# Performance work log

Hardware: AMD Instinct MI355X
Metric: run time of the kernel (lower is better)

The kernel has to match this reference:

```python
import jax, jax.numpy as jnp
import numpy as np

B, NV, NRINGS, NDIRS, C, F = 2, 20000, 8, 8, 16, 16


def setup_inputs() -> dict:
    key = jax.random.key(0)
    ks = jax.random.split(key, 7)
    y = jax.random.normal(ks[0], (B, NV, NDIRS, C), jnp.float32)
    contributors = jax.random.randint(ks[1], (NV, NRINGS, NDIRS, 3), 0, NV, dtype=jnp.int32)
    weights_bary = jax.random.uniform(ks[2], (NV, NRINGS, NDIRS, 3), jnp.float32)
    angles = jax.random.randint(ks[3], (NV, NRINGS, NDIRS, 3), 0, NDIRS, dtype=jnp.int32)
    kernel = jax.random.normal(ks[4], (NRINGS, NDIRS, C, F), jnp.float32) * 0.05
    center_kernel = jax.random.normal(ks[5], (C, F), jnp.float32) * 0.05
    bias = jnp.zeros((F,), jnp.float32)
    return {"y": y, "contributors": contributors, "weights_bary": weights_bary,
            "angles": angles, "kernel": kernel, "center_kernel": center_kernel, "bias": bias}


def reference(y, contributors, weights_bary, angles, kernel, center_kernel, bias):
    # y: (B, nv, ndirs, C); tables: (nv, nrings, ndirs, 3)
    b, nv, ndirs, nch = y.shape
    nfilters = kernel.shape[-1]
    nrings = contributors.shape[1]

    # window_interpolation_sync: gather 3 contributor vertices per window bin,
    # with the direction axis re-indexed per-contributor (radial sync), then
    # barycentric-weighted sum.  Flatten (vertex, dir) into one gather index.
    idx = contributors * ndirs + angles                 # (nv, nrings, ndirs, 3)
    y_flat = y.reshape(b, nv * ndirs, nch)
    gathered = y_flat[:, idx, :]                        # (B, nv, nrings, ndirs, 3, C)
    z = jnp.einsum('bvrdjc,vrdj->bvrdc', gathered, weights_bary)  # (B, nv, nrings, ndirs, C)

    # gcnn_conv: circular pad over dirs then VALID conv with (nrings, ndirs) kernel
    zr = z.reshape(b * nv, nrings, ndirs, nch)
    zr = jnp.concatenate([zr, zr[:, :, :-1, :]], axis=2)  # width 2*ndirs-1
    conv = jax.lax.conv_general_dilated(
        zr, kernel, window_strides=(1, 1), padding='VALID',
        dimension_numbers=('NHWC', 'HWIO', 'NHWC'))       # (B*nv, 1, ndirs, F)
    conv = conv.reshape(b, nv, ndirs, nfilters)

    out = conv + jnp.einsum('bvdc,cf->bvdf', y, center_kernel) + bias
    out = jax.nn.relu(out)
    return jnp.max(out, axis=2)                          # take_max over directions -> (B, nv, F)
```

## Files before the change

### kernel.cpp

```cpp
#include <hip/hip_runtime.h>

typedef unsigned short u16;
typedef __attribute__((ext_vector_type(4))) unsigned int u32x4;
typedef __attribute__((ext_vector_type(4))) float f32x4;
typedef __attribute__((ext_vector_type(8))) __bf16 bf16x8;

constexpr int BATCH = 2;
constexpr int NV    = 20000;
constexpr int ND    = 8;
constexpr int CH    = 16;
constexpr int NF    = 16;
constexpr int NVD   = NV * ND;
constexpr int NCHUNK = 36;
constexpr int MTOT  = BATCH * NV;
constexpr int BSTR  = 40;
constexpr int KSPLIT_CH = 18;
constexpr int PREP_BLOCKS = 1250;
constexpr int K2_BLOCKS   = (NCHUNK * 4096) / 256;

constexpr size_t Y16_OFF_B = 0;
constexpr size_t K2C_OFF_B = 10240000;
constexpr size_t PB_OFF_B  = 10534912;

__device__ __forceinline__ u16 f2bf(float x) {
    unsigned int u = __float_as_uint(x);
    unsigned int r = (u + 0x7fffu + ((u >> 16) & 1u)) >> 16;
    return (u16)r;
}
__device__ __forceinline__ unsigned int pack2bf(float a, float b) {
    return (unsigned int)f2bf(a) | ((unsigned int)f2bf(b) << 16);
}

__global__ __launch_bounds__(256) void prep_k2(const float* __restrict__ y,
                                               u16* __restrict__ y16,
                                               const float* __restrict__ kern,
                                               const float* __restrict__ ck,
                                               u16* __restrict__ k2c) {
    int bid = blockIdx.x;
    if (bid < PREP_BLOCKS) {
        int tid = bid * 256 + threadIdx.x;
        const float4* src = (const float4*)(y + (size_t)tid * 16);
        float4 v0 = src[0], v1 = src[1], v2 = src[2], v3 = src[3];
        u32x4 lo = {pack2bf(v0.x, v0.y), pack2bf(v0.z, v0.w), pack2bf(v1.x, v1.y), pack2bf(v1.z, v1.w)};
        u32x4 hi = {pack2bf(v2.x, v2.y), pack2bf(v2.z, v2.w), pack2bf(v3.x, v3.y), pack2bf(v3.z, v3.w)};
        u16* yd = y16 + (size_t)tid * 16;
        *(u32x4*)(yd)     = lo;
        *(u32x4*)(yd + 8) = hi;
    } else {
        int e = (bid - PREP_BLOCKS) * 256 + threadIdx.x;
        int i = e & 4095;
        int kc = e >> 12;
        int n = i >> 5, kk = i & 31;
        int k = kc * 32 + kk;
        int w = n >> 4, f = n & 15;
        float val;
        if (k < 1024) {
            int r = k >> 7, dd = (k >> 4) & 7, c = k & 15;
            int d = (dd - w) & 7;
            val = kern[((r * 8 + d) * 16 + c) * 16 + f];
        } else {
            int ke = k - 1024;
            int d = ke >> 4, c = ke & 15;
            val = (d == w) ? ck[c * 16 + f] : 0.f;
        }
        k2c[e] = f2bf(val);
    }
}

__global__ __launch_bounds__(256) void fused_gather_gemm(const u16* __restrict__ y16,
                                                         const int* __restrict__ contrib,
                                                         const float* __restrict__ wbary,
                                                         const int* __restrict__ angles,
                                                         const u16* __restrict__ k2c,
                                                         float* __restrict__ pb) {
    __shared__ __align__(16) u16 Bb[2][128 * BSTR];
    const int t = threadIdx.x;
    const int s  = blockIdx.x & 1;
    const int kcBeg = s * KSPLIT_CH;
    const int kcEnd = kcBeg + KSPLIT_CH;
    const int w = t >> 6, lane = t & 63;
    const int lrow = lane & 15, lq = lane >> 4;
    const int s_p = lq >> 1;
    const int h8  = (lq & 1) * 8;
    const int m0 = (blockIdx.x >> 1) * 64;
    const int arow = m0 + w * 16 + lrow;
    const int b_p = (arow >= NV);
    const int v_p = arow - b_p * NV;
    const u16* __restrict__ yb = y16 + (size_t)b_p * NVD * CH + h8;
    const int mb0 = v_p * 192 + s_p * 3;
    const int sn = t >> 1, sh = (t & 1) * 16;

    int   cA0, cA1, cA2, aA0, aA1, aA2;  float wA0, wA1, wA2, vA0, vA1, vA2;  u32x4 gA0, gA1, gA2;
    int   cB0, cB1, cB2, aB0, aB1, aB2;  float wB0, wB1, wB2, vB0, vB1, vB2;  u32x4 gB0, gB1, gB2;
    int   cC0, cC1, cC2, aC0, aC1, aC2;  float wC0, wC1, wC2, vC0, vC1, vC2;  u32x4 gC0, gC1, gC2;
    u32x4 bne0, bne1, bno0, bno1;

    f32x4 acc[8];
    #pragma unroll
    for (int nt = 0; nt < 8; ++nt) acc[nt] = (f32x4){0.f, 0.f, 0.f, 0.f};

#define META_ISSUE(S, KC_) { const int o_ = mb0 + (KC_) * 6;                       \
    c##S##0 = contrib[o_]; c##S##1 = contrib[o_ + 1]; c##S##2 = contrib[o_ + 2];   \
    a##S##0 = angles[o_];  a##S##1 = angles[o_ + 1];  a##S##2 = angles[o_ + 2];    \
    w##S##0 = wbary[o_];   w##S##1 = wbary[o_ + 1];   w##S##2 = wbary[o_ + 2]; }

#define G_ISSUE(S, KC_) {                                                          \
    if ((KC_) < 32) {                                                              \
        g##S##0 = *(const u32x4*)(yb + (size_t)((unsigned)c##S##0 * 128u +         \
                                                (unsigned)a##S##0 * 16u));         \
        g##S##1 = *(const u32x4*)(yb + (size_t)((unsigned)c##S##1 * 128u +         \
                                                (unsigned)a##S##1 * 16u));         \
        g##S##2 = *(const u32x4*)(yb + (size_t)((unsigned)c##S##2 * 128u +         \
                                                (unsigned)a##S##2 * 16u));         \
        v##S##0 = w##S##0; v##S##1 = w##S##1; v##S##2 = w##S##2;                   \
    } else {                                                                       \
        g##S##0 = *(const u32x4*)(yb + (size_t)((unsigned)v_p * 128u +             \
                                      (unsigned)(2 * ((KC_) - 32) + s_p) * 16u));  \
    } }

#define COMBINE(S, KC_, A_) {                                                      \
    if ((KC_) < 32) {                                                              \
        float ac_[8];                                                              \
        _Pragma("unroll") for (int x_ = 0; x_ < 8; ++x_) ac_[x_] = 0.f;            \
        _Pragma("unroll")                                                          \
        for (int q_ = 0; q_ < 4; ++q_) {                                           \
            unsigned u0_ = g##S##0[q_], u1_ = g##S##1[q_], u2_ = g##S##2[q_];      \
            ac_[2 * q_]     += v##S##0 * __uint_as_float(u0_ << 16);               \
            ac_[2 * q_ + 1] += v##S##0 * __uint_as_float(u0_ & 0xffff0000u);       \
            ac_[2 * q_]     += v##S##1 * __uint_as_float(u1_ << 16);               \
            ac_[2 * q_ + 1] += v##S##1 * __uint_as_float(u1_ & 0xffff0000u);       \
            ac_[2 * q_]     += v##S##2 * __uint_as_float(u2_ << 16);               \
            ac_[2 * q_ + 1] += v##S##2 * __uint_as_float(u2_ & 0xffff0000u);       \
        }                                                                          \
        u32x4 o_;                                                                  \
        _Pragma("unroll") for (int q_ = 0; q_ < 4; ++q_)                           \
            o_[q_] = pack2bf(ac_[2 * q_], ac_[2 * q_ + 1]);                        \
        A_ = *(bf16x8*)&o_;                                                        \
    } else { u32x4 o_ = g##S##0; A_ = *(bf16x8*)&o_; } }

#define CHUNK_EV(S, KC_) {                                                              \
    __syncthreads();                                                                    \
    if ((KC_) + 2 < kcEnd) {                                                            \
        const u32x4* src_ = (const u32x4*)(k2c + (size_t)((KC_) + 2) * 4096 + sn * 32 + sh); \
        bne0 = src_[0]; bne1 = src_[1];                                                 \
    }                                                                                   \
    bf16x8 av_;                                                                         \
    COMBINE(S, KC_, av_);                                                               \
    if ((KC_) + 3 < kcEnd) G_ISSUE(S, (KC_) + 3);                                       \
    if ((KC_) + 6 < kcEnd && (KC_) + 6 < 32) META_ISSUE(S, (KC_) + 6);                  \
    {   bf16x8 bf_[8];                                                                  \
        _Pragma("unroll")                                                               \
        for (int nt_ = 0; nt_ < 8; ++nt_)                                               \
            bf_[nt_] = *(const bf16x8*)(&Bb[0][(nt_ * 16 + lrow) * BSTR + lq * 8]);     \
        _Pragma("unroll")                                                               \
        for (int nt_ = 0; nt_ < 8; ++nt_)                                               \
            acc[nt_] = __builtin_amdgcn_mfma_f32_16x16x32_bf16(av_, bf_[nt_], acc[nt_], 0, 0, 0); \
    }                                                                                   \
    if ((KC_) + 1 < kcEnd) {                                                            \
        u16* dst_ = &Bb[1][sn * BSTR + sh];                                             \
        *(u32x4*)(dst_)     = bno0;                                                     \
        *(u32x4*)(dst_ + 8) = bno1;                                                     \
    } }

#define CHUNK_OD(S, KC_) {                                                              \
    __syncthreads();                                                                    \
    if ((KC_) + 2 < kcEnd) {                                                            \
        const u32x4* src_ = (const u32x4*)(k2c + (size_t)((KC_) + 2) * 4096 + sn * 32 + sh); \
        bno0 = src_[0]; bno1 = src_[1];                                                 \
    }                                                                                   \
    bf16x8 av_;                                                                         \
    COMBINE(S, KC_, av_);                                                               \
    if ((KC_) + 3 < kcEnd) G_ISSUE(S, (KC_) + 3);                                       \
    if ((KC_) + 6 < kcEnd && (KC_) + 6 < 32) META_ISSUE(S, (KC_) + 6);                  \
    {   bf16x8 bf_[8];                                                                  \
        _Pragma("unroll")                                                               \
        for (int nt_ = 0; nt_ < 8; ++nt_)                                               \
            bf_[nt_] = *(const bf16x8*)(&Bb[1][(nt_ * 16 + lrow) * BSTR + lq * 8]);     \
        _Pragma("unroll")                                                               \
        for (int nt_ = 0; nt_ < 8; ++nt_)                                               \
            acc[nt_] = __builtin_amdgcn_mfma_f32_16x16x32_bf16(av_, bf_[nt_], acc[nt_], 0, 0, 0); \
    }                                                                                   \
    if ((KC_) + 1 < kcEnd) {                                                            \
        u16* dst_ = &Bb[0][sn * BSTR + sh];                                             \
        *(u32x4*)(dst_)     = bne0;                                                     \
        *(u32x4*)(dst_ + 8) = bne1;                                                     \
    } }

    META_ISSUE(A, kcBeg + 0);
    META_ISSUE(B, kcBeg + 1);
    META_ISSUE(C, kcBeg + 2);
    {
        const u32x4* src = (const u32x4*)(k2c + (size_t)kcBeg * 4096 + sn * 32 + sh);
        u32x4 b0 = src[0], b1 = src[1];
        u16* dst = &Bb[0][sn * BSTR + sh];
        *(u32x4*)(dst)     = b0;
        *(u32x4*)(dst + 8) = b1;
    }
    G_ISSUE(A, kcBeg + 0); META_ISSUE(A, kcBeg + 3);
    G_ISSUE(B, kcBeg + 1); META_ISSUE(B, kcBeg + 4);
    G_ISSUE(C, kcBeg + 2); META_ISSUE(C, kcBeg + 5);
    {
        const u32x4* src = (const u32x4*)(k2c + (size_t)(kcBeg + 1) * 4096 + sn * 32 + sh);
        bno0 = src[0]; bno1 = src[1];
    }

    for (int p = 0; p < 3; ++p) {
        const int base = kcBeg + 6 * p;
        CHUNK_EV(A, base + 0);
        CHUNK_OD(B, base + 1);
        CHUNK_EV(C, base + 2);
        CHUNK_OD(A, base + 3);
        CHUNK_EV(B, base + 4);
        CHUNK_OD(C, base + 5);
    }
#undef META_ISSUE
#undef G_ISSUE
#undef COMBINE
#undef CHUNK_EV
#undef CHUNK_OD

    float* pbs = pb + (size_t)(s * 128) * MTOT;
    #pragma unroll
    for (int nt = 0; nt < 8; ++nt) {
        *(f32x4*)(pbs + (size_t)(nt * 16 + lrow) * MTOT + m0 + w * 16 + lq * 4) = acc[nt];
    }
}

__global__ __launch_bounds__(256) void combine_max(const float* __restrict__ pb,
                                                   const float* __restrict__ bias,
                                                   float* __restrict__ out) {
    int tid = blockIdx.x * 256 + threadIdx.x;
    if (tid >= 2 * MTOT) return;
    int row = tid >> 1, half = tid & 1;
    const float* p0 = pb + row;
    const float* p1 = pb + (size_t)128 * MTOT + row;
    float bs[8], m[8];
    #pragma unroll
    for (int j = 0; j < 8; ++j) { bs[j] = bias[half * 8 + j]; m[j] = 0.f; }
    #pragma unroll
    for (int w = 0; w < 8; ++w) {
        #pragma unroll
        for (int j = 0; j < 8; ++j) {
            int n = w * 16 + half * 8 + j;
            float v = p0[(size_t)n * MTOT] + p1[(size_t)n * MTOT] + bs[j];
            m[j] = fmaxf(m[j], v);
        }
    }
    float4 o0 = {m[0], m[1], m[2], m[3]};
    float4 o1 = {m[4], m[5], m[6], m[7]};
    float* dst = out + (size_t)row * NF + half * 8;
    *(float4*)(dst)     = o0;
    *(float4*)(dst + 4) = o1;
}

extern "C" void kernel_launch(void* const* d_in, const int* in_sizes, int n_in,
                              void* d_out, int out_size, void* d_ws, size_t ws_size,
                              hipStream_t stream) {
    const float* y      = (const float*)d_in[0];
    const int*   contrib= (const int*)d_in[1];
    const float* wbary  = (const float*)d_in[2];
    const int*   angles = (const int*)d_in[3];
    const float* kern   = (const float*)d_in[4];
    const float* ck     = (const float*)d_in[5];
    const float* bias   = (const float*)d_in[6];
    float* out = (float*)d_out;

    u16*   y16 = (u16*)((char*)d_ws + Y16_OFF_B);
    u16*   k2c = (u16*)((char*)d_ws + K2C_OFF_B);
    float* pb  = (float*)((char*)d_ws + PB_OFF_B);

    prep_k2<<<PREP_BLOCKS + K2_BLOCKS, 256, 0, stream>>>(y, y16, kern, ck, k2c);
    fused_gather_gemm<<<2 * (MTOT / 64), 256, 0, stream>>>(y16, contrib, wbary, angles,
                                                           k2c, pb);
    combine_max<<<(2 * MTOT + 255) / 256, 256, 0, stream>>>(pb, bias, out);
}
```

Baseline: 239.8 us.

## Precompute gather offsets and stage metadata through LDS with XCD-aware block mapping

A new prep pass fuses contributors and angles into a single precomputed element offset table. The GEMM kernel now loads that offset table and the barycentric weights cooperatively in coalesced int2/float2 form into double-buffered shared memory, so per-lane strided scalar metadata loads go away. Work items are remapped so each XCD's blocks handle one batch, which should keep that batch's y16 slice in the local L2. The cost is an extra 15MB write and read of the offset table in the prep kernel and extra LDS traffic and barriers.

```diff
diff --git a/kernel.cpp b/kernel.cpp
--- a/kernel.cpp
+++ b/kernel.cpp
@@ -15,12 +15,16 @@
 constexpr int MTOT  = BATCH * NV;
 constexpr int BSTR  = 40;
 constexpr int KSPLIT_CH = 18;
+constexpr int TPB   = 313;
+constexpr int ITEMS_PB = TPB * 2;
 constexpr int PREP_BLOCKS = 1250;
-constexpr int K2_BLOCKS   = (NCHUNK * 4096) / 256;
-
-constexpr size_t Y16_OFF_B = 0;
-constexpr size_t K2C_OFF_B = 10240000;
-constexpr size_t PB_OFF_B  = 10534912;
+constexpr int K2_BLOCKS   = 576;
+constexpr int MIDX_BLOCKS = 7500;
+
+constexpr size_t Y16_OFF_B  = 0;
+constexpr size_t K2C_OFF_B  = 10240000;
+constexpr size_t MIDX_OFF_B = 10534912;
+constexpr size_t PB_OFF_B   = 25894912;
 
 __device__ __forceinline__ u16 f2bf(float x) {
     unsigned int u = __float_as_uint(x);
@@ -35,7 +39,10 @@
                                                u16* __restrict__ y16,
                                                const float* __restrict__ kern,
                                                const float* __restrict__ ck,
-                                               u16* __restrict__ k2c) {
+                                               u16* __restrict__ k2c,
+                                               const int* __restrict__ contrib,
+                                               const int* __restrict__ angles,
+                                               int* __restrict__ midx) {
     int bid = blockIdx.x;
     if (bid < PREP_BLOCKS) {
         int tid = bid * 256 + threadIdx.x;
@@ -46,7 +53,7 @@
         u16* yd = y16 + (size_t)tid * 16;
         *(u32x4*)(yd)     = lo;
         *(u32x4*)(yd + 8) = hi;
-    } else {
+    } else if (bid < PREP_BLOCKS + K2_BLOCKS) {
         int e = (bid - PREP_BLOCKS) * 256 + threadIdx.x;
         int i = e & 4095;
         int kc = e >> 12;
@@ -64,59 +71,85 @@
             val = (d == w) ? ck[c * 16 + f] : 0.f;
         }
         k2c[e] = f2bf(val);
+    } else {
+        size_t k = (size_t)(bid - (PREP_BLOCKS + K2_BLOCKS)) * 256 + threadIdx.x;
+        int2 c = *(const int2*)(contrib + 2 * k);
+        int2 a = *(const int2*)(angles + 2 * k);
+        int2 m;
+        m.x = c.x * 128 + a.x * 16;
+        m.y = c.y * 128 + a.y * 16;
+        *(int2*)(midx + 2 * k) = m;
     }
 }
 
 __global__ __launch_bounds__(256) void fused_gather_gemm(const u16* __restrict__ y16,
-                                                         const int* __restrict__ contrib,
-                                                         const float* __restrict__ wbary,
-                                                         const int* __restrict__ angles,
+                                                         const int* __restrict__ midx,
+                                                         const float* __restrict__ wb,
                                                          const u16* __restrict__ k2c,
                                                          float* __restrict__ pb) {
     __shared__ __align__(16) u16 Bb[2][128 * BSTR];
+    __shared__ __align__(8) int   Mi[2][384];
+    __shared__ __align__(8) float Mw[2][384];
+    const int bid = blockIdx.x;
+    const int xcd = bid & 7;
+    const int g   = xcd >> 2;
+    const int item = (bid >> 3) * 4 + (xcd & 3);
+    if (item >= ITEMS_PB) return;
+    const int tile = item >> 1;
+    const int s    = item & 1;
+    const int kcBeg = s * KSPLIT_CH, kcEnd = kcBeg + KSPLIT_CH;
     const int t = threadIdx.x;
-    const int s  = blockIdx.x & 1;
-    const int kcBeg = s * KSPLIT_CH;
-    const int kcEnd = kcBeg + KSPLIT_CH;
     const int w = t >> 6, lane = t & 63;
     const int lrow = lane & 15, lq = lane >> 4;
     const int s_p = lq >> 1;
     const int h8  = (lq & 1) * 8;
-    const int m0 = (blockIdx.x >> 1) * 64;
-    const int arow = m0 + w * 16 + lrow;
-    const int b_p = (arow >= NV);
-    const int v_p = arow - b_p * NV;
-    const u16* __restrict__ yb = y16 + (size_t)b_p * NVD * CH + h8;
-    const int mb0 = v_p * 192 + s_p * 3;
+    const int rb  = tile * 64 + w * 16 + lrow;
+    const int v_p = rb < NV ? rb : NV - 1;
+    const int m0  = g * NV + tile * 64;
+    const u16* __restrict__ yb = y16 + (size_t)g * NVD * CH + h8;
     const int sn = t >> 1, sh = (t & 1) * 16;
-
-    int   cA0, cA1, cA2, aA0, aA1, aA2;  float wA0, wA1, wA2, vA0, vA1, vA2;  u32x4 gA0, gA1, gA2;
-    int   cB0, cB1, cB2, aB0, aB1, aB2;  float wB0, wB1, wB2, vB0, vB1, vB2;  u32x4 gB0, gB1, gB2;
-    int   cC0, cC1, cC2, aC0, aC1, aC2;  float wC0, wC1, wC2, vC0, vC1, vC2;  u32x4 gC0, gC1, gC2;
+    const bool stg = (t < 192);
+    const int stg_v = t / 3, stg_p = t % 3;
+    const int stg_vr = tile * 64 + stg_v;
+    const size_t stg_base = (size_t)(stg_vr < NV ? stg_vr : NV - 1) * 192 + stg_p * 2;
+    const int vloc6 = (w * 16 + lrow) * 6 + s_p * 3;
+
+    u32x4 gA0, gA1, gA2, gB0, gB1, gB2, gC0, gC1, gC2;
+    float vA0, vA1, vA2, vB0, vB1, vB2, vC0, vC1, vC2;
     u32x4 bne0, bne1, bno0, bno1;
+    int2   mi0, mi1;  float2 mw0, mw1;
 
     f32x4 acc[8];
     #pragma unroll
     for (int nt = 0; nt < 8; ++nt) acc[nt] = (f32x4){0.f, 0.f, 0.f, 0.f};
 
-#define META_ISSUE(S, KC_) { const int o_ = mb0 + (KC_) * 6;                       \
-    c##S##0 = contrib[o_]; c##S##1 = contrib[o_ + 1]; c##S##2 = contrib[o_ + 2];   \
-    a##S##0 = angles[o_];  a##S##1 = angles[o_ + 1];  a##S##2 = angles[o_ + 2];    \
-    w##S##0 = wbary[o_];   w##S##1 = wbary[o_ + 1];   w##S##2 = wbary[o_ + 2]; }
-
-#define G_ISSUE(S, KC_) {                                                          \
+#define MLOAD(SET, KC_) if (stg && (KC_) < 32 && (KC_) < kcEnd) {                  \
+    mi##SET = *(const int2*)(midx + stg_base + (size_t)(KC_) * 6);                 \
+    mw##SET = *(const float2*)(wb + stg_base + (size_t)(KC_) * 6); }
+
+#define MWRITE(SET, P_, KC_) if (stg && (KC_) < 32 && (KC_) < kcEnd) {             \
+    *(int2*)(&Mi[P_][stg_v * 6 + stg_p * 2]) = mi##SET;                            \
+    *(float2*)(&Mw[P_][stg_v * 6 + stg_p * 2]) = mw##SET; }
+
+#define G_LDS(S, KC_, P_) {                                                        \
     if ((KC_) < 32) {                                                              \
-        g##S##0 = *(const u32x4*)(yb + (size_t)((unsigned)c##S##0 * 128u +         \
-                                                (unsigned)a##S##0 * 16u));         \
-        g##S##1 = *(const u32x4*)(yb + (size_t)((unsigned)c##S##1 * 128u +         \
-                                                (unsigned)a##S##1 * 16u));         \
-        g##S##2 = *(const u32x4*)(yb + (size_t)((unsigned)c##S##2 * 128u +         \
-                                                (unsigned)a##S##2 * 16u));         \
-        v##S##0 = w##S##0; v##S##1 = w##S##1; v##S##2 = w##S##2;                   \
+        const int i0_ = Mi[P_][vloc6], i1_ = Mi[P_][vloc6 + 1], i2_ = Mi[P_][vloc6 + 2]; \
+        v##S##0 = Mw[P_][vloc6]; v##S##1 = Mw[P_][vloc6 + 1]; v##S##2 = Mw[P_][vloc6 + 2]; \
+        g##S##0 = *(const u32x4*)(yb + (unsigned)i0_);                             \
+        g##S##1 = *(const u32x4*)(yb + (unsigned)i1_);                             \
+        g##S##2 = *(const u32x4*)(yb + (unsigned)i2_);                             \
     } else {                                                                       \
         g##S##0 = *(const u32x4*)(yb + (size_t)((unsigned)v_p * 128u +             \
                                       (unsigned)(2 * ((KC_) - 32) + s_p) * 16u));  \
     } }
+
+#define PRO_G(S, KC_) {                                                            \
+    size_t mo_ = (size_t)v_p * 192 + (KC_) * 6 + s_p * 3;                          \
+    const int i0_ = midx[mo_], i1_ = midx[mo_ + 1], i2_ = midx[mo_ + 2];           \
+    v##S##0 = wb[mo_]; v##S##1 = wb[mo_ + 1]; v##S##2 = wb[mo_ + 2];               \
+    g##S##0 = *(const u32x4*)(yb + (unsigned)i0_);                                 \
+    g##S##1 = *(const u32x4*)(yb + (unsigned)i1_);                                 \
+    g##S##2 = *(const u32x4*)(yb + (unsigned)i2_); }
 
 #define COMBINE(S, KC_, A_) {                                                      \
     if ((KC_) < 32) {                                                              \
@@ -140,14 +173,15 @@
 
 #define CHUNK_EV(S, KC_) {                                                              \
     __syncthreads();                                                                    \
+    MLOAD(1, (KC_) + 5)                                                                 \
     if ((KC_) + 2 < kcEnd) {                                                            \
         const u32x4* src_ = (const u32x4*)(k2c + (size_t)((KC_) + 2) * 4096 + sn * 32 + sh); \
         bne0 = src_[0]; bne1 = src_[1];                                                 \
     }                                                                                   \
     bf16x8 av_;                                                                         \
     COMBINE(S, KC_, av_);                                                               \
-    if ((KC_) + 3 < kcEnd) G_ISSUE(S, (KC_) + 3);                                       \
-    if ((KC_) + 6 < kcEnd && (KC_) + 6 < 32) META_ISSUE(S, (KC_) + 6);                  \
+    if ((KC_) + 3 < kcEnd) G_LDS(S, (KC_) + 3, 1)                                       \
+    MWRITE(0, 0, (KC_) + 4)                                                             \
     {   bf16x8 bf_[8];                                                                  \
         _Pragma("unroll")                                                               \
         for (int nt_ = 0; nt_ < 8; ++nt_)                                               \
@@ -156,22 +190,22 @@
         for (int nt_ = 0; nt_ < 8; ++nt_)                                               \
             acc[nt_] = __builtin_amdgcn_mfma_f32_16x16x32_bf16(av_, bf_[nt_], acc[nt_], 0, 0, 0); \
     }                                                                                   \
-    if ((KC_) + 1 < kcEnd) {                                                            \
-        u16* dst_ = &Bb[1][sn * BSTR + sh];                                             \
+    {   u16* dst_ = &Bb[1][sn * BSTR + sh];                                             \
         *(u32x4*)(dst_)     = bno0;                                                     \
         *(u32x4*)(dst_ + 8) = bno1;                                                     \
     } }
 
 #define CHUNK_OD(S, KC_) {                                                              \
     __syncthreads();                                                                    \
+    MLOAD(0, (KC_) + 5)                                                                 \
     if ((KC_) + 2 < kcEnd) {                                                            \
         const u32x4* src_ = (const u32x4*)(k2c + (size_t)((KC_) + 2) * 4096 + sn * 32 + sh); \
         bno0 = src_[0]; bno1 = src_[1];                                                 \
     }                                                                                   \
     bf16x8 av_;                                                                         \
     COMBINE(S, KC_, av_);                                                               \
-    if ((KC_) + 3 < kcEnd) G_ISSUE(S, (KC_) + 3);                                       \
-    if ((KC_) + 6 < kcEnd && (KC_) + 6 < 32) META_ISSUE(S, (KC_) + 6);                  \
+    if ((KC_) + 3 < kcEnd) G_LDS(S, (KC_) + 3, 0)                                       \
+    MWRITE(1, 1, (KC_) + 4)                                                             \
     {   bf16x8 bf_[8];                                                                  \
         _Pragma("unroll")                                                               \
         for (int nt_ = 0; nt_ < 8; ++nt_)                                               \
@@ -186,9 +220,9 @@
         *(u32x4*)(dst_ + 8) = bne1;                                                     \
     } }
 
-    META_ISSUE(A, kcBeg + 0);
-    META_ISSUE(B, kcBeg + 1);
-    META_ISSUE(C, kcBeg + 2);
+    PRO_G(A, kcBeg + 0);
+    PRO_G(B, kcBeg + 1);
+    PRO_G(C, kcBeg + 2);
     {
         const u32x4* src = (const u32x4*)(k2c + (size_t)kcBeg * 4096 + sn * 32 + sh);
         u32x4 b0 = src[0], b1 = src[1];
@@ -196,9 +230,13 @@
         *(u32x4*)(dst)     = b0;
         *(u32x4*)(dst + 8) = b1;
     }
-    G_ISSUE(A, kcBeg + 0); META_ISSUE(A, kcBeg + 3);
-    G_ISSUE(B, kcBeg + 1); META_ISSUE(B, kcBeg + 4);
-    G_ISSUE(C, kcBeg + 2); META_ISSUE(C, kcBeg + 5);
+    if (stg) {
+        int2   tmi = *(const int2*)(midx + stg_base + (size_t)(kcBeg + 3) * 6);
+        float2 tmw = *(const float2*)(wb + stg_base + (size_t)(kcBeg + 3) * 6);
+        *(int2*)(&Mi[1][stg_v * 6 + stg_p * 2]) = tmi;
+        *(float2*)(&Mw[1][stg_v * 6 + stg_p * 2]) = tmw;
+    }
+    MLOAD(0, kcBeg + 4)
     {
         const u32x4* src = (const u32x4*)(k2c + (size_t)(kcBeg + 1) * 4096 + sn * 32 + sh);
         bno0 = src[0]; bno1 = src[1];
@@ -213,16 +251,21 @@
         CHUNK_EV(B, base + 4);
         CHUNK_OD(C, base + 5);
     }
-#undef META_ISSUE
-#undef G_ISSUE
+#undef MLOAD
+#undef MWRITE
+#undef G_LDS
+#undef PRO_G
 #undef COMBINE
 #undef CHUNK_EV
 #undef CHUNK_OD
 
-    float* pbs = pb + (size_t)(s * 128) * MTOT;
-    #pragma unroll
-    for (int nt = 0; nt < 8; ++nt) {
-        *(f32x4*)(pbs + (size_t)(nt * 16 + lrow) * MTOT + m0 + w * 16 + lq * 4) = acc[nt];
+    const bool mval = (tile * 64 + w * 16 + lq * 4) < NV;
+    if (mval) {
+        float* pbs = pb + (size_t)(s * 128) * MTOT;
+        #pragma unroll
+        for (int nt = 0; nt < 8; ++nt) {
+            *(f32x4*)(pbs + (size_t)(nt * 16 + lrow) * MTOT + m0 + w * 16 + lq * 4) = acc[nt];
+        }
     }
 }
 
@@ -265,12 +308,13 @@
     const float* bias   = (const float*)d_in[6];
     float* out = (float*)d_out;
 
-    u16*   y16 = (u16*)((char*)d_ws + Y16_OFF_B);
-    u16*   k2c = (u16*)((char*)d_ws + K2C_OFF_B);
-    float* pb  = (float*)((char*)d_ws + PB_OFF_B);
-
-    prep_k2<<<PREP_BLOCKS + K2_BLOCKS, 256, 0, stream>>>(y, y16, kern, ck, k2c);
-    fused_gather_gemm<<<2 * (MTOT / 64), 256, 0, stream>>>(y16, contrib, wbary, angles,
-                                                           k2c, pb);
+    u16*   y16  = (u16*)((char*)d_ws + Y16_OFF_B);
+    u16*   k2c  = (u16*)((char*)d_ws + K2C_OFF_B);
+    int*   midx = (int*)((char*)d_ws + MIDX_OFF_B);
+    float* pb   = (float*)((char*)d_ws + PB_OFF_B);
+
+    prep_k2<<<PREP_BLOCKS + K2_BLOCKS + MIDX_BLOCKS, 256, 0, stream>>>(
+        y, y16, kern, ck, k2c, contrib, angles, midx);
+    fused_gather_gemm<<<1256, 256, 0, stream>>>(y16, midx, wbary, k2c, pb);
     combine_max<<<(2 * MTOT + 255) / 256, 256, 0, stream>>>(pb, bias, out);
 }
```

After: 216.8 us. 9.6% less time.
